# Kernel optimization log

Hardware: AMD Instinct MI355X
Metric: run time of the kernel (lower is better)

## Reference

```python
import jax, jax.numpy as jnp
import numpy as np

D_MODEL, D_FF, N_EXPERTS, TOP_K = 1024, 4096, 8, 2


def setup_inputs() -> dict:
    key = jax.random.key(0)
    k1, k2, k3, k4 = jax.random.split(key, 4)
    x = jax.random.normal(k1, (2, 2048, D_MODEL), dtype=jnp.float32)
    Wg = jax.random.normal(k2, (D_MODEL, N_EXPERTS), dtype=jnp.float32) * 0.02
    W1 = jax.random.normal(k3, (N_EXPERTS, D_MODEL, D_FF), dtype=jnp.float32) * 0.02
    b1 = jnp.zeros((N_EXPERTS, D_FF), dtype=jnp.float32)
    W2 = jax.random.normal(k4, (N_EXPERTS, D_FF, D_MODEL), dtype=jnp.float32) * 0.02
    b2 = jnp.zeros((N_EXPERTS, D_MODEL), dtype=jnp.float32)
    return {"x": x, "Wg": Wg, "W1": W1, "b1": b1, "W2": W2, "b2": b2}


def reference(x, Wg, W1, b1, W2, b2):
    B, S, D = x.shape
    T = B * S
    flat_x = x.reshape(T, D)                      # [T, D]
    # Router: softmax over expert logits, keep top-k experts per token.
    logits = flat_x @ Wg                          # [T, E]
    probs = jax.nn.softmax(logits, axis=-1)       # [T, E]
    _, top_idx = jax.lax.top_k(probs, TOP_K)      # [T, K]
    # mask[t, e] = 1 if expert e is among token t's top-k
    mask = jax.nn.one_hot(top_idx, N_EXPERTS, dtype=probs.dtype).sum(axis=1)  # [T, E]
    weights = probs * mask                        # gating score only for routed experts
    # Dense grouped expert MLP: every expert applied to all tokens, then masked-combined.
    h = jax.nn.gelu(jnp.einsum('td,edh->eth', flat_x, W1) + b1[:, None, :])  # [E, T, H]
    y = jnp.einsum('eth,ehd->etd', h, W2) + b2[:, None, :]                   # [E, T, D]
    out = jnp.einsum('etd,te->td', y, weights)                               # [T, D]
    return out.reshape(B, S, D)
```

## Files before the change

### kernel.cpp

```cpp
#include <hip/hip_runtime.h>
#include <hip/hip_bf16.h>

#define D_MODEL 1024
#define D_FF    4096
#define N_EXPERTS 8
#define TOPK    2
#define T_TOK   4096
#define NPAIR   (T_TOK * TOPK)
#define MT_MAX  32

typedef __attribute__((ext_vector_type(8))) short s8v;
typedef __attribute__((ext_vector_type(4))) float f4v;
typedef __attribute__((ext_vector_type(4))) unsigned short u16x4;
typedef __attribute__((ext_vector_type(8))) unsigned short u16x8;

__device__ __forceinline__ void async16(const void* g, void* l) {
    __builtin_amdgcn_global_load_lds(
        (const __attribute__((address_space(1))) void*)g,
        (__attribute__((address_space(3))) void*)l, 16, 0, 0);
}

__device__ __forceinline__ float gelu_tanh(float v) {
    float u = 0.7978845608028654f * (v + 0.044715f * v * v * v);
    float t = 1.0f - 2.0f / (1.0f + __expf(2.0f * u));
    return 0.5f * v * (1.0f + t);
}

__device__ __forceinline__ unsigned short f2bf(float f) {
    union { __hip_bfloat16 b; unsigned short u; } cv;
    cv.b = __float2bfloat16(f);
    return cv.u;
}

__global__ __launch_bounds__(256) void router_kernel(
    const float* __restrict__ x, const float* __restrict__ Wg,
    int* __restrict__ top_e, float* __restrict__ top_w,
    __hip_bfloat16* __restrict__ xb)
{
    int wave = threadIdx.x >> 6;
    int lane = threadIdx.x & 63;
    int t = blockIdx.x * 4 + wave;
    if (t >= T_TOK) return;

    float acc[8] = {0.f,0.f,0.f,0.f,0.f,0.f,0.f,0.f};
    const float* xr = x + (size_t)t * D_MODEL;
    unsigned short* xbr = (unsigned short*)xb + (size_t)t * D_MODEL;
    #pragma unroll
    for (int it = 0; it < 4; it++) {
        int d0 = it * 256 + lane * 4;
        float4 xv = *(const float4*)(xr + d0);
        unsigned short bfv[4] = {f2bf(xv.x), f2bf(xv.y), f2bf(xv.z), f2bf(xv.w)};
        *(u16x4*)(xbr + d0) = *(u16x4*)bfv;
        float xa[4] = {xv.x, xv.y, xv.z, xv.w};
        #pragma unroll
        for (int u = 0; u < 4; u++) {
            const float* wr = Wg + (size_t)(d0 + u) * N_EXPERTS;
            float4 w0 = *(const float4*)wr;
            float4 w1 = *(const float4*)(wr + 4);
            acc[0] += xa[u] * w0.x; acc[1] += xa[u] * w0.y;
            acc[2] += xa[u] * w0.z; acc[3] += xa[u] * w0.w;
            acc[4] += xa[u] * w1.x; acc[5] += xa[u] * w1.y;
            acc[6] += xa[u] * w1.z; acc[7] += xa[u] * w1.w;
        }
    }
    #pragma unroll
    for (int off = 32; off >= 1; off >>= 1) {
        #pragma unroll
        for (int e = 0; e < 8; e++) acc[e] += __shfl_xor(acc[e], off);
    }
    if (lane == 0) {
        float m = acc[0];
        #pragma unroll
        for (int e = 1; e < 8; e++) m = fmaxf(m, acc[e]);
        float p[8]; float s = 0.f;
        #pragma unroll
        for (int e = 0; e < 8; e++) { p[e] = expf(acc[e] - m); s += p[e]; }
        float inv = 1.f / s;
        #pragma unroll
        for (int e = 0; e < 8; e++) p[e] *= inv;
        int i0 = 0; float b0 = p[0];
        #pragma unroll
        for (int e = 1; e < 8; e++) if (p[e] > b0) { b0 = p[e]; i0 = e; }
        int i1 = -1; float b1 = -1.f;
        #pragma unroll
        for (int e = 0; e < 8; e++) if (e != i0 && p[e] > b1) { b1 = p[e]; i1 = e; }
        top_e[2*t]   = i0; top_w[2*t]   = b0;
        top_e[2*t+1] = i1; top_w[2*t+1] = b1;
    }
}

__global__ __launch_bounds__(256) void setup_kernel(
    const int* __restrict__ top_e, int* __restrict__ offsets,
    int* __restrict__ pair_id)
{
    __shared__ int cnt[N_EXPERTS], base[N_EXPERTS], cur[N_EXPERTS];
    int tid = threadIdx.x;
    if (tid < N_EXPERTS) { cnt[tid] = 0; cur[tid] = 0; }
    __syncthreads();
    for (int i = tid; i < NPAIR; i += 256) atomicAdd(&cnt[top_e[i]], 1);
    __syncthreads();
    if (tid == 0) {
        int run = 0;
        #pragma unroll
        for (int e = 0; e < N_EXPERTS; e++) { base[e] = run; offsets[e] = run; run += cnt[e]; }
        offsets[N_EXPERTS] = run;
    }
    __syncthreads();
    for (int i = tid; i < NPAIR; i += 256) {
        int e = top_e[i];
        int pos = atomicAdd(&cur[e], 1);
        pair_id[base[e] + pos] = i;
    }
}

__global__ __launch_bounds__(256) void transpose_cast_kernel(
    const float* __restrict__ src, __hip_bfloat16* __restrict__ dst, int R, int C)
{
    int e = blockIdx.z;
    src += (size_t)e * R * C;
    dst += (size_t)e * R * C;
    int b0 = blockIdx.x * 64;
    int a0 = blockIdx.y * 64;

    __shared__ float tile[64][65];
    int tid = threadIdx.x;
    int lr = tid >> 4;
    int lc = (tid & 15) * 4;
    #pragma unroll
    for (int rr = 0; rr < 4; rr++) {
        int r = lr + rr * 16;
        *(float4*)&tile[r][lc] = *(const float4*)(src + (size_t)(a0 + r) * C + b0 + lc);
    }
    __syncthreads();
    int oc = tid >> 3;
    int oj = (tid & 7) * 8;
    #pragma unroll
    for (int rr = 0; rr < 2; rr++) {
        int c = oc + rr * 32;
        unsigned short t[8];
        #pragma unroll
        for (int j = 0; j < 8; j++) t[j] = f2bf(tile[oj + j][c]);
        *(u16x8*)((unsigned short*)dst + (size_t)(b0 + c) * R + a0 + oj) = *(u16x8*)t;
    }
}

__global__ __launch_bounds__(256) void gemm1_mfma(
    const __hip_bfloat16* __restrict__ xb, const __hip_bfloat16* __restrict__ W1T,
    const float* __restrict__ b1,
    const int* __restrict__ offsets, const int* __restrict__ pair_id,
    __hip_bfloat16* __restrict__ h)
{
    int e  = blockIdx.y >> 5;
    int mt = blockIdx.y & 31;
    int off_e = offsets[e];
    int cnt   = offsets[e + 1] - off_e;
    int m0 = mt * 128;
    if (m0 >= cnt) return;
    int n0 = blockIdx.x * 128;

    __shared__ __hip_bfloat16 As[128 * 32];
    __shared__ __hip_bfloat16 Bs[128 * 32];
    __shared__ int pid[128];

    int tid = threadIdx.x;
    if (tid < 128) {
        int r = m0 + tid; if (r >= cnt) r = cnt - 1;
        pid[tid] = pair_id[off_e + r];
    }
    __syncthreads();

    int lane = tid & 63, wid = tid >> 6;
    int c0 = tid, c1 = tid + 256;
    int r0 = ((c0 >> 6) << 4) | (c0 & 15), kb0 = (c0 >> 4) & 3;
    int r1 = ((c1 >> 6) << 4) | (c1 & 15), kb1 = (c1 >> 4) & 3;

    const __hip_bfloat16* gA0 = xb + (size_t)(pid[r0] >> 1) * D_MODEL + kb0 * 8;
    const __hip_bfloat16* gA1 = xb + (size_t)(pid[r1] >> 1) * D_MODEL + kb1 * 8;
    const __hip_bfloat16* WT  = W1T + (size_t)e * (D_MODEL * D_FF);
    const __hip_bfloat16* gB0 = WT + (size_t)(n0 + r0) * D_MODEL + kb0 * 8;
    const __hip_bfloat16* gB1 = WT + (size_t)(n0 + r1) * D_MODEL + kb1 * 8;

    int fm = lane & 15;
    int wm = (wid >> 1) * 64;
    int wn = (wid & 1) * 64;
    int rba = (wid >> 1) * 4;
    int rbb = (wid & 1) * 4;

    f4v acc[4][4];
    #pragma unroll
    for (int i = 0; i < 4; i++)
        #pragma unroll
        for (int j = 0; j < 4; j++)
            acc[i][j] = (f4v){0.f, 0.f, 0.f, 0.f};

    for (int k0 = 0; k0 < D_MODEL; k0 += 32) {
        async16(gA0 + k0, As + c0 * 8);
        async16(gA1 + k0, As + c1 * 8);
        async16(gB0 + k0, Bs + c0 * 8);
        async16(gB1 + k0, Bs + c1 * 8);
        __syncthreads();
        s8v af[4], bfr[4];
        #pragma unroll
        for (int i = 0; i < 4; i++)
            af[i] = *(const s8v*)(As + (rba + i) * 512 + lane * 8);
        #pragma unroll
        for (int j = 0; j < 4; j++)
            bfr[j] = *(const s8v*)(Bs + (rbb + j) * 512 + lane * 8);
        #pragma unroll
        for (int i = 0; i < 4; i++)
            #pragma unroll
            for (int j = 0; j < 4; j++)
                acc[i][j] = __builtin_amdgcn_mfma_f32_16x16x32_bf16(af[i], bfr[j], acc[i][j], 0, 0, 0);
        __syncthreads();
    }

    int rq = (lane >> 4) * 4;
    #pragma unroll
    for (int i = 0; i < 4; i++) {
        #pragma unroll
        for (int j = 0; j < 4; j++) {
            int n = n0 + wn + j * 16 + fm;
            float bias = b1[e * D_FF + n];
            #pragma unroll
            for (int r = 0; r < 4; r++) {
                int m = wm + i * 16 + rq + r;
                if (m0 + m < cnt) {
                    float v = acc[i][j][r] + bias;
                    h[(size_t)(off_e + m0 + m) * D_FF + n] = __float2bfloat16(gelu_tanh(v));
                }
            }
        }
    }
}

__global__ __launch_bounds__(256) void gemm2_mfma(
    const __hip_bfloat16* __restrict__ h, const __hip_bfloat16* __restrict__ W2T,
    const float* __restrict__ b2,
    const int* __restrict__ offsets, const int* __restrict__ pair_id,
    float* __restrict__ y)
{
    int e  = blockIdx.y >> 5;
    int mt = blockIdx.y & 31;
    int off_e = offsets[e];
    int cnt   = offsets[e + 1] - off_e;
    int m0 = mt * 128;
    if (m0 >= cnt) return;
    int n0 = blockIdx.x * 128;

    __shared__ __hip_bfloat16 As[128 * 32];
    __shared__ __hip_bfloat16 Bs[128 * 32];
    __shared__ int pid[128];

    int tid = threadIdx.x;
    if (tid < 128) {
        int r = m0 + tid; if (r >= cnt) r = cnt - 1;
        pid[tid] = pair_id[off_e + r];
    }
    __syncthreads();

    int lane = tid & 63, wid = tid >> 6;
    int c0 = tid, c1 = tid + 256;
    int r0 = ((c0 >> 6) << 4) | (c0 & 15), kb0 = (c0 >> 4) & 3;
    int r1 = ((c1 >> 6) << 4) | (c1 & 15), kb1 = (c1 >> 4) & 3;
    int mr0 = m0 + r0; if (mr0 >= cnt) mr0 = cnt - 1;
    int mr1 = m0 + r1; if (mr1 >= cnt) mr1 = cnt - 1;

    const __hip_bfloat16* gA0 = h + (size_t)(off_e + mr0) * D_FF + kb0 * 8;
    const __hip_bfloat16* gA1 = h + (size_t)(off_e + mr1) * D_FF + kb1 * 8;
    const __hip_bfloat16* WT  = W2T + (size_t)e * (D_FF * D_MODEL);
    const __hip_bfloat16* gB0 = WT + (size_t)(n0 + r0) * D_FF + kb0 * 8;
    const __hip_bfloat16* gB1 = WT + (size_t)(n0 + r1) * D_FF + kb1 * 8;

    int fm = lane & 15;
    int wm = (wid >> 1) * 64;
    int wn = (wid & 1) * 64;
    int rba = (wid >> 1) * 4;
    int rbb = (wid & 1) * 4;

    f4v acc[4][4];
    #pragma unroll
    for (int i = 0; i < 4; i++)
        #pragma unroll
        for (int j = 0; j < 4; j++)
            acc[i][j] = (f4v){0.f, 0.f, 0.f, 0.f};

    for (int k0 = 0; k0 < D_FF; k0 += 32) {
        async16(gA0 + k0, As + c0 * 8);
        async16(gA1 + k0, As + c1 * 8);
        async16(gB0 + k0, Bs + c0 * 8);
        async16(gB1 + k0, Bs + c1 * 8);
        __syncthreads();
        s8v af[4], bfr[4];
        #pragma unroll
        for (int i = 0; i < 4; i++)
            af[i] = *(const s8v*)(As + (rba + i) * 512 + lane * 8);
        #pragma unroll
        for (int j = 0; j < 4; j++)
            bfr[j] = *(const s8v*)(Bs + (rbb + j) * 512 + lane * 8);
        #pragma unroll
        for (int i = 0; i < 4; i++)
            #pragma unroll
            for (int j = 0; j < 4; j++)
                acc[i][j] = __builtin_amdgcn_mfma_f32_16x16x32_bf16(af[i], bfr[j], acc[i][j], 0, 0, 0);
        __syncthreads();
    }

    int rq = (lane >> 4) * 4;
    #pragma unroll
    for (int i = 0; i < 4; i++) {
        #pragma unroll
        for (int j = 0; j < 4; j++) {
            int n = n0 + wn + j * 16 + fm;
            float bias = b2[e * D_MODEL + n];
            #pragma unroll
            for (int r = 0; r < 4; r++) {
                int m = wm + i * 16 + rq + r;
                if (m0 + m < cnt) {
                    int p = pid[m];
                    y[(size_t)p * D_MODEL + n] = acc[i][j][r] + bias;
                }
            }
        }
    }
}

__global__ __launch_bounds__(256) void combine_kernel(
    const float* __restrict__ y, const float* __restrict__ top_w,
    float* __restrict__ out)
{
    int gid = blockIdx.x * blockDim.x + threadIdx.x;
    int t = gid >> 8;
    int c = gid & 255;
    float w0 = top_w[2*t];
    float w1 = top_w[2*t + 1];
    const float4* y0 = (const float4*)(y + (size_t)(2*t) * D_MODEL);
    const float4* y1 = (const float4*)(y + (size_t)(2*t + 1) * D_MODEL);
    float4 a = y0[c], b = y1[c];
    float4 o;
    o.x = w0*a.x + w1*b.x; o.y = w0*a.y + w1*b.y;
    o.z = w0*a.z + w1*b.z; o.w = w0*a.w + w1*b.w;
    ((float4*)out)[gid] = o;
}

extern "C" void kernel_launch(void* const* d_in, const int* in_sizes, int n_in,
                              void* d_out, int out_size, void* d_ws, size_t ws_size,
                              hipStream_t stream)
{
    const float* x  = (const float*)d_in[0];
    const float* Wg = (const float*)d_in[1];
    const float* W1 = (const float*)d_in[2];
    const float* b1 = (const float*)d_in[3];
    const float* W2 = (const float*)d_in[4];
    const float* b2 = (const float*)d_in[5];
    float* out = (float*)d_out;

    char* ws = (char*)d_ws;
    size_t off = 0;
    int*   top_e   = (int*)(ws + off);  off += (size_t)NPAIR * 4;
    float* top_w   = (float*)(ws + off); off += (size_t)NPAIR * 4;
    int*   offsets = (int*)(ws + off);  off += 256;
    int*   pair_id = (int*)(ws + off);  off += (size_t)NPAIR * 4;
    off = (off + 255) & ~(size_t)255;
    __hip_bfloat16* xb  = (__hip_bfloat16*)(ws + off); off += (size_t)T_TOK * D_MODEL * 2;
    __hip_bfloat16* W1T = (__hip_bfloat16*)(ws + off); off += (size_t)N_EXPERTS * D_MODEL * D_FF * 2;
    __hip_bfloat16* W2T = (__hip_bfloat16*)(ws + off); off += (size_t)N_EXPERTS * D_MODEL * D_FF * 2;
    __hip_bfloat16* h   = (__hip_bfloat16*)(ws + off); off += (size_t)NPAIR * D_FF * 2;
    float*          y   = (float*)(ws + off);          off += (size_t)NPAIR * D_MODEL * 4;

    router_kernel<<<T_TOK / 4, 256, 0, stream>>>(x, Wg, top_e, top_w, xb);
    setup_kernel<<<1, 256, 0, stream>>>(top_e, offsets, pair_id);

    transpose_cast_kernel<<<dim3(D_FF / 64, D_MODEL / 64, N_EXPERTS), 256, 0, stream>>>(
        W1, W1T, D_MODEL, D_FF);
    transpose_cast_kernel<<<dim3(D_MODEL / 64, D_FF / 64, N_EXPERTS), 256, 0, stream>>>(
        W2, W2T, D_FF, D_MODEL);

    gemm1_mfma<<<dim3(D_FF / 128, N_EXPERTS * MT_MAX), 256, 0, stream>>>(
        xb, W1T, b1, offsets, pair_id, h);
    gemm2_mfma<<<dim3(D_MODEL / 128, N_EXPERTS * MT_MAX), 256, 0, stream>>>(
        h, W2T, b2, offsets, pair_id, y);
    combine_kernel<<<T_TOK, 256, 0, stream>>>(y, top_w, out);
}
```

Baseline: 719.9 us.

## Double-buffer LDS tiles in both expert GEMMs and halve GEMM2 M-tile

```diff
diff --git a/kernel.cpp b/kernel.cpp
--- a/kernel.cpp
+++ b/kernel.cpp
@@ -8,6 +8,7 @@
 #define T_TOK   4096
 #define NPAIR   (T_TOK * TOPK)
 #define MT_MAX  32
+#define MT2_MAX 64
 
 typedef __attribute__((ext_vector_type(8))) short s8v;
 typedef __attribute__((ext_vector_type(4))) float f4v;
@@ -158,8 +159,8 @@
     if (m0 >= cnt) return;
     int n0 = blockIdx.x * 128;
 
-    __shared__ __hip_bfloat16 As[128 * 32];
-    __shared__ __hip_bfloat16 Bs[128 * 32];
+    __shared__ __hip_bfloat16 As[2][128 * 32];
+    __shared__ __hip_bfloat16 Bs[2][128 * 32];
     __shared__ int pid[128];
 
     int tid = threadIdx.x;
@@ -193,25 +194,47 @@
         for (int j = 0; j < 4; j++)
             acc[i][j] = (f4v){0.f, 0.f, 0.f, 0.f};
 
-    for (int k0 = 0; k0 < D_MODEL; k0 += 32) {
-        async16(gA0 + k0, As + c0 * 8);
-        async16(gA1 + k0, As + c1 * 8);
-        async16(gB0 + k0, Bs + c0 * 8);
-        async16(gB1 + k0, Bs + c1 * 8);
-        __syncthreads();
+    async16(gA0, As[0] + c0 * 8);
+    async16(gA1, As[0] + c1 * 8);
+    async16(gB0, Bs[0] + c0 * 8);
+    async16(gB1, Bs[0] + c1 * 8);
+    __syncthreads();
+
+    int cur = 0;
+    for (int k0 = 32; k0 < D_MODEL; k0 += 32) {
+        int nxt = cur ^ 1;
+        async16(gA0 + k0, As[nxt] + c0 * 8);
+        async16(gA1 + k0, As[nxt] + c1 * 8);
+        async16(gB0 + k0, Bs[nxt] + c0 * 8);
+        async16(gB1 + k0, Bs[nxt] + c1 * 8);
         s8v af[4], bfr[4];
         #pragma unroll
         for (int i = 0; i < 4; i++)
-            af[i] = *(const s8v*)(As + (rba + i) * 512 + lane * 8);
-        #pragma unroll
-        for (int j = 0; j < 4; j++)
-            bfr[j] = *(const s8v*)(Bs + (rbb + j) * 512 + lane * 8);
+            af[i] = *(const s8v*)(As[cur] + (rba + i) * 512 + lane * 8);
+        #pragma unroll
+        for (int j = 0; j < 4; j++)
+            bfr[j] = *(const s8v*)(Bs[cur] + (rbb + j) * 512 + lane * 8);
         #pragma unroll
         for (int i = 0; i < 4; i++)
             #pragma unroll
             for (int j = 0; j < 4; j++)
                 acc[i][j] = __builtin_amdgcn_mfma_f32_16x16x32_bf16(af[i], bfr[j], acc[i][j], 0, 0, 0);
         __syncthreads();
+        cur = nxt;
+    }
+    {
+        s8v af[4], bfr[4];
+        #pragma unroll
+        for (int i = 0; i < 4; i++)
+            af[i] = *(const s8v*)(As[cur] + (rba + i) * 512 + lane * 8);
+        #pragma unroll
+        for (int j = 0; j < 4; j++)
+            bfr[j] = *(const s8v*)(Bs[cur] + (rbb + j) * 512 + lane * 8);
+        #pragma unroll
+        for (int i = 0; i < 4; i++)
+            #pragma unroll
+            for (int j = 0; j < 4; j++)
+                acc[i][j] = __builtin_amdgcn_mfma_f32_16x16x32_bf16(af[i], bfr[j], acc[i][j], 0, 0, 0);
     }
 
     int rq = (lane >> 4) * 4;
@@ -239,75 +262,93 @@
     const int* __restrict__ offsets, const int* __restrict__ pair_id,
     float* __restrict__ y)
 {
-    int e  = blockIdx.y >> 5;
-    int mt = blockIdx.y & 31;
+    int e  = blockIdx.y >> 6;
+    int mt = blockIdx.y & 63;
     int off_e = offsets[e];
     int cnt   = offsets[e + 1] - off_e;
-    int m0 = mt * 128;
+    int m0 = mt * 64;
     if (m0 >= cnt) return;
     int n0 = blockIdx.x * 128;
 
-    __shared__ __hip_bfloat16 As[128 * 32];
-    __shared__ __hip_bfloat16 Bs[128 * 32];
-    __shared__ int pid[128];
+    __shared__ __hip_bfloat16 As[2][64 * 32];
+    __shared__ __hip_bfloat16 Bs[2][128 * 32];
+    __shared__ int pid[64];
 
     int tid = threadIdx.x;
-    if (tid < 128) {
+    if (tid < 64) {
         int r = m0 + tid; if (r >= cnt) r = cnt - 1;
         pid[tid] = pair_id[off_e + r];
     }
-    __syncthreads();
 
     int lane = tid & 63, wid = tid >> 6;
     int c0 = tid, c1 = tid + 256;
     int r0 = ((c0 >> 6) << 4) | (c0 & 15), kb0 = (c0 >> 4) & 3;
     int r1 = ((c1 >> 6) << 4) | (c1 & 15), kb1 = (c1 >> 4) & 3;
+
     int mr0 = m0 + r0; if (mr0 >= cnt) mr0 = cnt - 1;
-    int mr1 = m0 + r1; if (mr1 >= cnt) mr1 = cnt - 1;
 
     const __hip_bfloat16* gA0 = h + (size_t)(off_e + mr0) * D_FF + kb0 * 8;
-    const __hip_bfloat16* gA1 = h + (size_t)(off_e + mr1) * D_FF + kb1 * 8;
     const __hip_bfloat16* WT  = W2T + (size_t)e * (D_FF * D_MODEL);
     const __hip_bfloat16* gB0 = WT + (size_t)(n0 + r0) * D_FF + kb0 * 8;
     const __hip_bfloat16* gB1 = WT + (size_t)(n0 + r1) * D_FF + kb1 * 8;
 
     int fm = lane & 15;
-    int wm = (wid >> 1) * 64;
+    int wm = (wid >> 1) * 32;
     int wn = (wid & 1) * 64;
-    int rba = (wid >> 1) * 4;
+    int rba = (wid >> 1) * 2;
     int rbb = (wid & 1) * 4;
 
-    f4v acc[4][4];
-    #pragma unroll
-    for (int i = 0; i < 4; i++)
+    f4v acc[2][4];
+    #pragma unroll
+    for (int i = 0; i < 2; i++)
         #pragma unroll
         for (int j = 0; j < 4; j++)
             acc[i][j] = (f4v){0.f, 0.f, 0.f, 0.f};
 
-    for (int k0 = 0; k0 < D_FF; k0 += 32) {
-        async16(gA0 + k0, As + c0 * 8);
-        async16(gA1 + k0, As + c1 * 8);
-        async16(gB0 + k0, Bs + c0 * 8);
-        async16(gB1 + k0, Bs + c1 * 8);
-        __syncthreads();
-        s8v af[4], bfr[4];
-        #pragma unroll
-        for (int i = 0; i < 4; i++)
-            af[i] = *(const s8v*)(As + (rba + i) * 512 + lane * 8);
-        #pragma unroll
-        for (int j = 0; j < 4; j++)
-            bfr[j] = *(const s8v*)(Bs + (rbb + j) * 512 + lane * 8);
-        #pragma unroll
-        for (int i = 0; i < 4; i++)
+    async16(gA0, As[0] + c0 * 8);
+    async16(gB0, Bs[0] + c0 * 8);
+    async16(gB1, Bs[0] + c1 * 8);
+    __syncthreads();
+
+    int cur = 0;
+    for (int k0 = 32; k0 < D_FF; k0 += 32) {
+        int nxt = cur ^ 1;
+        async16(gA0 + k0, As[nxt] + c0 * 8);
+        async16(gB0 + k0, Bs[nxt] + c0 * 8);
+        async16(gB1 + k0, Bs[nxt] + c1 * 8);
+        s8v af[2], bfr[4];
+        #pragma unroll
+        for (int i = 0; i < 2; i++)
+            af[i] = *(const s8v*)(As[cur] + (rba + i) * 512 + lane * 8);
+        #pragma unroll
+        for (int j = 0; j < 4; j++)
+            bfr[j] = *(const s8v*)(Bs[cur] + (rbb + j) * 512 + lane * 8);
+        #pragma unroll
+        for (int i = 0; i < 2; i++)
             #pragma unroll
             for (int j = 0; j < 4; j++)
                 acc[i][j] = __builtin_amdgcn_mfma_f32_16x16x32_bf16(af[i], bfr[j], acc[i][j], 0, 0, 0);
         __syncthreads();
+        cur = nxt;
+    }
+    {
+        s8v af[2], bfr[4];
+        #pragma unroll
+        for (int i = 0; i < 2; i++)
+            af[i] = *(const s8v*)(As[cur] + (rba + i) * 512 + lane * 8);
+        #pragma unroll
+        for (int j = 0; j < 4; j++)
+            bfr[j] = *(const s8v*)(Bs[cur] + (rbb + j) * 512 + lane * 8);
+        #pragma unroll
+        for (int i = 0; i < 2; i++)
+            #pragma unroll
+            for (int j = 0; j < 4; j++)
+                acc[i][j] = __builtin_amdgcn_mfma_f32_16x16x32_bf16(af[i], bfr[j], acc[i][j], 0, 0, 0);
     }
 
     int rq = (lane >> 4) * 4;
     #pragma unroll
-    for (int i = 0; i < 4; i++) {
+    for (int i = 0; i < 2; i++) {
         #pragma unroll
         for (int j = 0; j < 4; j++) {
             int n = n0 + wn + j * 16 + fm;
@@ -377,7 +418,7 @@
 
     gemm1_mfma<<<dim3(D_FF / 128, N_EXPERTS * MT_MAX), 256, 0, stream>>>(
         xb, W1T, b1, offsets, pair_id, h);
-    gemm2_mfma<<<dim3(D_MODEL / 128, N_EXPERTS * MT_MAX), 256, 0, stream>>>(
+    gemm2_mfma<<<dim3(D_MODEL / 128, N_EXPERTS * MT2_MAX), 256, 0, stream>>>(
         h, W2T, b2, offsets, pair_id, y);
     combine_kernel<<<T_TOK, 256, 0, stream>>>(y, top_w, out);
 }
```

After: 766.1 us. 6.4% more time.
